# Kernel tuning notes

Hardware: AMD Instinct MI355X
Metric: run time of the kernel (lower is better)

The kernel has to match this reference:

```python
import jax, jax.numpy as jnp
import numpy as np

B, T, D, K = 64, 4096, 128, 512

def setup_inputs() -> dict:
    key = jax.random.key(0)
    k1, k2, k3 = jax.random.split(key, 3)
    embeddings = jax.random.normal(k1, (B, T, D), dtype=jnp.float32)
    mask = jax.random.bernoulli(k2, 0.9, (B, T))
    W = jax.random.normal(k3, (D,), dtype=jnp.float32) * (1.0 / np.sqrt(D))
    b = jnp.zeros((1,), dtype=jnp.float32)
    return {"embeddings": embeddings, "mask": mask, "k": K, "W": W, "b": b}

def reference(embeddings, mask, k, W, b):
    batch, T, dim = embeddings.shape
    if k >= T:
        return embeddings, mask
    # linear score head: (B,T,D) @ (D,) + b -> (B,T)
    scores = jnp.einsum("btd,d->bt", embeddings, W) + b[0]
    neg_inf = jnp.array(-jnp.inf, dtype=scores.dtype)
    scores = jnp.where(mask, scores, neg_inf)
    soft_scores = jax.nn.sigmoid(scores)  # sigmoid(-inf) == 0
    _, topk_idx = jax.lax.top_k(scores, k)          # (B, k)
    topk_idx_sorted = jnp.sort(topk_idx, axis=1)    # preserve original token order
    rows = jnp.arange(batch)[:, None]
    hard_mask = jnp.zeros_like(scores).at[rows, topk_idx].set(1.0)
    # straight-through estimator: hard forward, soft gradient
    ste_mask = hard_mask - jax.lax.stop_gradient(soft_scores) + soft_scores
    weighted = embeddings * ste_mask[:, :, None]
    selected = jnp.take_along_axis(weighted, topk_idx_sorted[:, :, None], axis=1)  # (B,k,D)
    selected_mask = jnp.take_along_axis(mask, topk_idx_sorted, axis=1)             # (B,k)
    return selected, selected_mask
```

## Files before the change

### kernel.cpp

```cpp
#include <hip/hip_runtime.h>
#include <hip/hip_bf16.h>

#define BB 64
#define TT 4096
#define DD 128
#define KK 512

__global__ __launch_bounds__(256) void k_scores(
    const float* __restrict__ emb, const int* __restrict__ mask,
    const float* __restrict__ W, const float* __restrict__ bias,
    float* __restrict__ scores)
{
    const int wave = threadIdx.x >> 6;
    const int lane = threadIdx.x & 63;
    const int token0 = (blockIdx.x * 4 + wave) * 16;

    const float2 w = ((const float2*)W)[lane];
    const double wx = (double)w.x, wy = (double)w.y;
    const double b0 = (double)bias[0];

    for (int i = 0; i < 16; ++i) {
        const int t = token0 + i;
        const float2 e = ((const float2*)emb)[(size_t)t * 64 + lane];
        double s = (double)e.x * wx + (double)e.y * wy;
        s += __shfl_xor(s, 32, 64);
        s += __shfl_xor(s, 16, 64);
        s += __shfl_xor(s,  8, 64);
        s += __shfl_xor(s,  4, 64);
        s += __shfl_xor(s,  2, 64);
        s += __shfl_xor(s,  1, 64);
        if (lane == 0) {
            const float val = (float)(s + b0);
            scores[t] = mask[t] ? val : __uint_as_float(0xFF800000u);
        }
    }
}

__global__ __launch_bounds__(256) void k_select(
    const float* __restrict__ scores, const int* __restrict__ mask,
    int* __restrict__ idx_out, float* __restrict__ mask_out)
{
    __shared__ unsigned int keys[TT];
    __shared__ unsigned int hist[256];
    __shared__ unsigned int scanbuf[256];
    __shared__ unsigned int bcast[2];

    const int row = blockIdx.x;
    const int tid = threadIdx.x;
    const float* srow = scores + (size_t)row * TT;
    const int*   mrow = mask   + (size_t)row * TT;

    for (int i = 0; i < 16; ++i) {
        const int t = tid * 16 + i;
        const unsigned int u = __float_as_uint(srow[t]);
        keys[t] = (u & 0x80000000u) ? ~u : (u | 0x80000000u);
    }
    __syncthreads();

    unsigned int prefix = 0;
    unsigned int count_above = 0;
    for (int pass = 0; pass < 4; ++pass) {
        const int shift = 24 - 8 * pass;
        hist[tid] = 0;
        __syncthreads();
        for (int i = 0; i < 16; ++i) {
            const unsigned int k = keys[tid * 16 + i];
            const bool in_group = (pass == 0) || ((k >> (shift + 8)) == prefix);
            if (in_group) atomicAdd(&hist[(k >> shift) & 0xFFu], 1u);
        }
        __syncthreads();
        const unsigned int histv = hist[tid];
        unsigned int v = histv;
        scanbuf[tid] = v;
        __syncthreads();
        for (int off = 1; off < 256; off <<= 1) {
            const unsigned int add = (tid + off < 256) ? scanbuf[tid + off] : 0u;
            __syncthreads();
            v += add;
            scanbuf[tid] = v;
            __syncthreads();
        }
        const unsigned int excl = v - histv;
        if (count_above + v >= KK && count_above + excl < KK) {
            bcast[0] = (unsigned int)tid;
            bcast[1] = count_above + excl;
        }
        __syncthreads();
        prefix = (prefix << 8) | bcast[0];
        count_above = bcast[1];
        __syncthreads();
    }
    const unsigned int vstar = prefix;
    const unsigned int need  = KK - count_above;

    unsigned int gt = 0, eq = 0;
    for (int i = 0; i < 16; ++i) {
        const unsigned int k = keys[tid * 16 + i];
        gt += (k > vstar);
        eq += (k == vstar);
    }
    const unsigned int packed = (gt << 16) | eq;
    scanbuf[tid] = packed;
    __syncthreads();
    unsigned int v2 = packed;
    for (int off = 1; off < 256; off <<= 1) {
        const unsigned int add = (tid >= off) ? scanbuf[tid - off] : 0u;
        __syncthreads();
        v2 += add;
        scanbuf[tid] = v2;
        __syncthreads();
    }
    const unsigned int before = v2 - packed;
    unsigned int gt_b = before >> 16;
    unsigned int eq_b = before & 0xFFFFu;
    for (int i = 0; i < 16; ++i) {
        const int t = tid * 16 + i;
        const unsigned int k = keys[t];
        if (k > vstar) {
            const unsigned int pos = gt_b + (eq_b < need ? eq_b : need);
            idx_out[row * KK + pos]  = t;
            mask_out[row * KK + pos] = mrow[t] ? 1.0f : 0.0f;
            gt_b++;
        } else if (k == vstar) {
            if (eq_b < need) {
                const unsigned int pos = gt_b + eq_b;
                idx_out[row * KK + pos]  = t;
                mask_out[row * KK + pos] = mrow[t] ? 1.0f : 0.0f;
            }
            eq_b++;
        }
    }
}

__global__ __launch_bounds__(256) void k_gather(
    const float* __restrict__ emb, const int* __restrict__ idx,
    float* __restrict__ out)
{
    const int gp   = blockIdx.x * 8 + (threadIdx.x >> 5);
    const int lane = threadIdx.x & 31;
    const int b = gp >> 9;
    const int t = idx[gp];
    const float4* src = (const float4*)(emb + ((size_t)b * TT + t) * DD);
    float4*       dst = (float4*)(out + (size_t)gp * DD);
    dst[lane] = src[lane];
}

extern "C" void kernel_launch(void* const* d_in, const int* in_sizes, int n_in,
                              void* d_out, int out_size, void* d_ws, size_t ws_size,
                              hipStream_t stream)
{
    const float* emb  = (const float*)d_in[0];
    const int*   mask = (const int*)d_in[1];
    const float* W    = (const float*)d_in[3];
    const float* bias = (const float*)d_in[4];

    float* out_sel  = (float*)d_out;
    float* out_mask = (float*)d_out + (size_t)BB * KK * DD;

    float* scores = (float*)d_ws;
    int*   idx    = (int*)((char*)d_ws + (size_t)BB * TT * sizeof(float));

    k_scores<<<BB * TT / 64, 256, 0, stream>>>(emb, mask, W, bias, scores);
    k_select<<<BB, 256, 0, stream>>>(scores, mask, idx, out_mask);
    k_gather<<<BB * KK / 8, 256, 0, stream>>>(emb, idx, out_sel);
}
```

Measured before the change: 235.0 us.

## Use wave-shuffle scans and per-wave histograms in top-k select; widen score loads

Replaces the shared-memory Hillis-Steele scans in the radix select kernel with a wave-level shuffle scan plus a small cross-wave sum, cutting the number of block barriers per pass. Histogram atomics go to per-wave copies to reduce LDS contention. The descending scan order is now done by reversing bin indices. The scores kernel loads float4 per lane and handles two tokens per wave-iteration. The initial barrier after filling keys is removed, but the first pass's barrier after clearing the histograms still precedes any reads.

```diff
diff --git a/kernel.cpp b/kernel.cpp
--- a/kernel.cpp
+++ b/kernel.cpp
@@ -13,27 +13,48 @@
 {
     const int wave = threadIdx.x >> 6;
     const int lane = threadIdx.x & 63;
-    const int token0 = (blockIdx.x * 4 + wave) * 16;
+    const int half = lane >> 5;
+    const int sub  = lane & 31;
+    const int pair0 = (blockIdx.x * 4 + wave) * 8;
 
-    const float2 w = ((const float2*)W)[lane];
-    const double wx = (double)w.x, wy = (double)w.y;
+    const float4 w = ((const float4*)W)[sub];
+    const double w0 = (double)w.x, w1 = (double)w.y, w2 = (double)w.z, w3 = (double)w.w;
     const double b0 = (double)bias[0];
 
-    for (int i = 0; i < 16; ++i) {
-        const int t = token0 + i;
-        const float2 e = ((const float2*)emb)[(size_t)t * 64 + lane];
-        double s = (double)e.x * wx + (double)e.y * wy;
-        s += __shfl_xor(s, 32, 64);
+#pragma unroll
+    for (int i = 0; i < 8; ++i) {
+        const int t = (pair0 + i) * 2 + half;
+        const float4 e = ((const float4*)emb)[(size_t)t * 32 + sub];
+        double s = (double)e.x * w0 + (double)e.y * w1
+                 + (double)e.z * w2 + (double)e.w * w3;
         s += __shfl_xor(s, 16, 64);
         s += __shfl_xor(s,  8, 64);
         s += __shfl_xor(s,  4, 64);
         s += __shfl_xor(s,  2, 64);
         s += __shfl_xor(s,  1, 64);
-        if (lane == 0) {
+        if (sub == 0) {
             const float val = (float)(s + b0);
             scores[t] = mask[t] ? val : __uint_as_float(0xFF800000u);
         }
     }
+}
+
+__device__ __forceinline__ unsigned int block_incl_prefix(
+    unsigned int v, int tid, volatile unsigned int* wsum)
+{
+    const int lane = tid & 63, wv = tid >> 6;
+#pragma unroll
+    for (int off = 1; off < 64; off <<= 1) {
+        const unsigned int u = __shfl_up(v, off, 64);
+        if (lane >= off) v += u;
+    }
+    if (lane == 63) wsum[wv] = v;
+    __syncthreads();
+    unsigned int add = 0;
+    for (int w = 0; w < wv; ++w) add += wsum[w];
+    v += add;
+    __syncthreads();
+    return v;
 }
 
 __global__ __launch_bounds__(256) void k_select(
@@ -41,48 +62,44 @@
     int* __restrict__ idx_out, float* __restrict__ mask_out)
 {
     __shared__ unsigned int keys[TT];
-    __shared__ unsigned int hist[256];
-    __shared__ unsigned int scanbuf[256];
+    __shared__ unsigned int hist4[4][256];
+    __shared__ unsigned int wsum[4];
     __shared__ unsigned int bcast[2];
 
     const int row = blockIdx.x;
     const int tid = threadIdx.x;
+    const int wv  = tid >> 6;
     const float* srow = scores + (size_t)row * TT;
     const int*   mrow = mask   + (size_t)row * TT;
 
+#pragma unroll
     for (int i = 0; i < 16; ++i) {
         const int t = tid * 16 + i;
         const unsigned int u = __float_as_uint(srow[t]);
         keys[t] = (u & 0x80000000u) ? ~u : (u | 0x80000000u);
     }
-    __syncthreads();
 
     unsigned int prefix = 0;
     unsigned int count_above = 0;
     for (int pass = 0; pass < 4; ++pass) {
         const int shift = 24 - 8 * pass;
-        hist[tid] = 0;
+#pragma unroll
+        for (int w = 0; w < 4; ++w) hist4[w][tid] = 0;
         __syncthreads();
+#pragma unroll
         for (int i = 0; i < 16; ++i) {
             const unsigned int k = keys[tid * 16 + i];
             const bool in_group = (pass == 0) || ((k >> (shift + 8)) == prefix);
-            if (in_group) atomicAdd(&hist[(k >> shift) & 0xFFu], 1u);
+            if (in_group) atomicAdd(&hist4[wv][(k >> shift) & 0xFFu], 1u);
         }
         __syncthreads();
-        const unsigned int histv = hist[tid];
-        unsigned int v = histv;
-        scanbuf[tid] = v;
-        __syncthreads();
-        for (int off = 1; off < 256; off <<= 1) {
-            const unsigned int add = (tid + off < 256) ? scanbuf[tid + off] : 0u;
-            __syncthreads();
-            v += add;
-            scanbuf[tid] = v;
-            __syncthreads();
-        }
-        const unsigned int excl = v - histv;
-        if (count_above + v >= KK && count_above + excl < KK) {
-            bcast[0] = (unsigned int)tid;
+        const unsigned int bin = 255u - (unsigned int)tid;
+        const unsigned int h = hist4[0][bin] + hist4[1][bin]
+                             + hist4[2][bin] + hist4[3][bin];
+        const unsigned int incl = block_incl_prefix(h, tid, wsum);
+        const unsigned int excl = incl - h;
+        if (count_above + incl >= KK && count_above + excl < KK) {
+            bcast[0] = bin;
             bcast[1] = count_above + excl;
         }
         __syncthreads();
@@ -94,25 +111,18 @@
     const unsigned int need  = KK - count_above;
 
     unsigned int gt = 0, eq = 0;
+#pragma unroll
     for (int i = 0; i < 16; ++i) {
         const unsigned int k = keys[tid * 16 + i];
         gt += (k > vstar);
         eq += (k == vstar);
     }
     const unsigned int packed = (gt << 16) | eq;
-    scanbuf[tid] = packed;
-    __syncthreads();
-    unsigned int v2 = packed;
-    for (int off = 1; off < 256; off <<= 1) {
-        const unsigned int add = (tid >= off) ? scanbuf[tid - off] : 0u;
-        __syncthreads();
-        v2 += add;
-        scanbuf[tid] = v2;
-        __syncthreads();
-    }
-    const unsigned int before = v2 - packed;
+    const unsigned int incl2 = block_incl_prefix(packed, tid, wsum);
+    const unsigned int before = incl2 - packed;
     unsigned int gt_b = before >> 16;
     unsigned int eq_b = before & 0xFFFFu;
+#pragma unroll
     for (int i = 0; i < 16; ++i) {
         const int t = tid * 16 + i;
         const unsigned int k = keys[t];
```

New measurement: 219.7 us. -6.5%, faster.
